# Optimization experiments

Measured on AMD Instinct MI355X. Metric: run time of the kernel, lower is better.

Reference implementation:

```python
import jax, jax.numpy as jnp
import numpy as np

N_QUBITS = 12
DIM = 2 ** N_QUBITS
BATCH = 2048


def setup_inputs() -> dict:
    key = jax.random.key(0)
    k1, k2, k3 = jax.random.split(key, 3)
    inputs = jax.random.normal(k1, (BATCH, N_QUBITS), dtype=jnp.float32)
    weight = jax.random.normal(k2, (3 + 2 * N_QUBITS,), dtype=jnp.float32)
    entangle_matrix = jax.random.normal(k3, (DIM, DIM), dtype=jnp.float32)
    return {"inputs": inputs, "weight": weight, "entangle_matrix": entangle_matrix}


def _encode(ry_angles, rz_angles):
    # Encoder: state = prod over qubits of first column of (Rz*Ry) per qubit.
    ry = ry_angles / 2
    rz = rz_angles / 2
    a = jnp.cos(ry) * jnp.exp(-1j * rz)  # entry11 (row bit = 0)
    b = jnp.sin(ry) * jnp.exp(1j * rz)   # entry21 (row bit = 1)
    col2 = jnp.stack([a, b], axis=-1).astype(jnp.complex64)  # [B, n, 2]
    B, n = ry.shape
    v = jnp.ones((B, 1), dtype=jnp.complex64)
    for q in range(n):  # Kronecker fold over qubits (big-endian, matches dec2bin)
        v = (v[:, :, None] * col2[:, q][:, None, :]).reshape(B, -1)
    return v  # [B, 2^n]


def _rot_mat(w):
    # rot_mat: per-qubit Rx(w[q]) @ Rz(w[n+q]), then full Kronecker product.
    n = w.shape[0] // 2
    tx = (w[:n] / 2).astype(jnp.complex64)
    tz = (w[n:] / 2).astype(jnp.complex64)
    c, s = jnp.cos(tx), jnp.sin(tx)
    rx = jnp.stack([jnp.stack([c, -1j * s], -1),
                    jnp.stack([-1j * s, c], -1)], -2)  # [n,2,2]
    ez = jnp.exp(-1j * tz)
    zero = jnp.zeros_like(ez)
    rz = jnp.stack([jnp.stack([ez, zero], -1),
                    jnp.stack([zero, jnp.exp(1j * tz)], -1)], -2)  # [n,2,2]
    mats = jnp.einsum('qij,qjk->qik', rx, rz)
    M = mats[0]
    for q in range(1, n):
        M = jnp.kron(M, mats[q])
    return M  # [2^n, 2^n]


def _ry2(theta):
    a = theta / 2
    c, s = jnp.cos(a), jnp.sin(a)
    return jnp.stack([jnp.stack([c, -s]), jnp.stack([s, c])])  # [2,2] real


def _final_rot(th3):
    # final_rot_mat: Rz-form @ Ry-form @ Rx-form (all ry_mat_list), kron with identity.
    rot = _ry2(th3[2]) @ (_ry2(th3[1]) @ _ry2(th3[0]))
    eye = jnp.eye(DIM // 2, dtype=jnp.complex64)
    return jnp.kron(rot.astype(jnp.complex64), eye)  # [DIM, DIM]


def reference(inputs, weight, entangle_matrix):
    # initial=False branch
    ry_angles = inputs
    rz_angles = jnp.square(inputs)
    v = _encode(ry_angles, rz_angles)                 # [B, DIM] complex64
    E = entangle_matrix.astype(jnp.complex64)
    R = _rot_mat(weight[3:])
    M = E @ R @ E                                     # [DIM, DIM]
    v = v @ M.T                                       # tensordot dims ([-1],[-1])
    F = _final_rot(weight[:3])
    v = v @ F.T
    half = DIM // 2
    # vector[:, half:] = 0 then sum |.|^2  <=>  sum over first half
    return jnp.sum(jnp.square(jnp.abs(v[:, :half])), axis=-1)  # [B] float32
```

## Files before the change

kernel.cpp:

```cpp
#include <hip/hip_runtime.h>
#include <math.h>

#define QDIM 4096
#define NQ 12
#define QBATCH 2048

typedef _Float16 f16x8 __attribute__((ext_vector_type(8)));
typedef float f32x4 __attribute__((ext_vector_type(4)));
typedef int i32x4 __attribute__((ext_vector_type(4)));

__device__ __forceinline__ void gld_lds16(const void* gptr, void* ldsptr) {
    __builtin_amdgcn_global_load_lds(
        (const __attribute__((address_space(1))) void*)gptr,
        (__attribute__((address_space(3))) void*)ldsptr,
        16, 0, 0);
}

__device__ __forceinline__ int q8(float x) {
    float y = fminf(fmaxf(x, -127.f), 127.f);
    return (int)rintf(y);
}
__device__ __forceinline__ int pack4_i8(int a, int b, int c, int d) {
    return (a & 0xFF) | ((b & 0xFF) << 8) | ((c & 0xFF) << 16) | ((d & 0xFF) << 24);
}

__global__ __launch_bounds__(256) void conv_kernel(
    const float* __restrict__ E, const float* __restrict__ wgt,
    _Float16* __restrict__ Eh, signed char* __restrict__ G8)
{
    float th = 0.5f * (wgt[0] + wgt[1] + wgt[2]);
    float c0 = cosf(th), c1 = -sinf(th);
    const float qs = 127.f / 6.f;
    size_t flat = ((size_t)blockIdx.x * 256 + threadIdx.x) * 8;
    size_t n = flat >> 12;
    size_t k = flat & (QDIM - 1);
    const float* p0 = E + n * QDIM + k;
    const float* p1 = p0 + (size_t)QBATCH * QDIM;
    float4 a0 = ((const float4*)p0)[0], a1 = ((const float4*)p0)[1];
    float4 b0 = ((const float4*)p1)[0], b1 = ((const float4*)p1)[1];
    f16x8 h0 = { (_Float16)a0.x, (_Float16)a0.y, (_Float16)a0.z, (_Float16)a0.w,
                 (_Float16)a1.x, (_Float16)a1.y, (_Float16)a1.z, (_Float16)a1.w };
    f16x8 h1 = { (_Float16)b0.x, (_Float16)b0.y, (_Float16)b0.z, (_Float16)b0.w,
                 (_Float16)b1.x, (_Float16)b1.y, (_Float16)b1.z, (_Float16)b1.w };
    *(f16x8*)&Eh[n * QDIM + k] = h0;
    *(f16x8*)&Eh[(n + QBATCH) * QDIM + k] = h1;
    float g[8] = { c0*a0.x + c1*b0.x, c0*a0.y + c1*b0.y, c0*a0.z + c1*b0.z, c0*a0.w + c1*b0.w,
                   c0*a1.x + c1*b1.x, c0*a1.y + c1*b1.y, c0*a1.z + c1*b1.z, c0*a1.w + c1*b1.w };
    int2 gp = { pack4_i8(q8(g[0]*qs), q8(g[1]*qs), q8(g[2]*qs), q8(g[3]*qs)),
                pack4_i8(q8(g[4]*qs), q8(g[5]*qs), q8(g[6]*qs), q8(g[7]*qs)) };
    *(int2*)&G8[n * QDIM + k] = gp;
}

__global__ __launch_bounds__(256) void expand_kernel(
    const float* __restrict__ inputs, _Float16* __restrict__ A1,
    float* __restrict__ out)
{
    __shared__ float ab[NQ][4];
    const int b = blockIdx.x;
    const int tid = threadIdx.x;
    if (tid == 0) out[b] = 0.f;
    if (tid < NQ) {
        float x = inputs[b * NQ + tid];
        float ry = 0.5f * x;
        float rz = 0.5f * x * x;
        float ca = cosf(ry), sa = sinf(ry), cz = cosf(rz), sz = sinf(rz);
        ab[tid][0] = ca * cz;  ab[tid][1] = -ca * sz;
        ab[tid][2] = sa * cz;  ab[tid][3] =  sa * sz;
    }
    __syncthreads();
    float pr0 = 1.f, pi0 = 0.f;
#pragma unroll
    for (int q = 0; q < 8; ++q) {
        int bit = (tid >> (7 - q)) & 1;
        float cr = ab[q][bit * 2 + 0], ci = ab[q][bit * 2 + 1];
        float nr = pr0 * cr - pi0 * ci;
        float ni = pr0 * ci + pi0 * cr;
        pr0 = nr; pi0 = ni;
    }
    f16x8 vr[2], vi[2];
#pragma unroll
    for (int u = 0; u < 16; ++u) {
        float pr = pr0, pi = pi0;
#pragma unroll
        for (int q = 8; q < 12; ++q) {
            int bit = (u >> (11 - q)) & 1;
            float cr = ab[q][bit * 2 + 0], ci = ab[q][bit * 2 + 1];
            float nr = pr * cr - pi * ci;
            float ni = pr * ci + pi * cr;
            pr = nr; pi = ni;
        }
        vr[u >> 3][u & 7] = (_Float16)pr;
        vi[u >> 3][u & 7] = (_Float16)pi;
    }
    const int idx0 = tid * 16;
    *(f16x8*)&A1[(size_t)b * QDIM + idx0] = vr[0];
    *(f16x8*)&A1[(size_t)b * QDIM + idx0 + 8] = vr[1];
    *(f16x8*)&A1[(size_t)(b + QBATCH) * QDIM + idx0] = vi[0];
    *(f16x8*)&A1[(size_t)(b + QBATCH) * QDIM + idx0 + 8] = vi[1];
}

__global__ __launch_bounds__(256) void gemm_f16(
    const _Float16* __restrict__ A, const _Float16* __restrict__ B,
    _Float16* __restrict__ C, int N)
{
    const int K = QDIM;
    __shared__ __attribute__((aligned(16))) _Float16 As[128 * 64];
    __shared__ __attribute__((aligned(16))) _Float16 Bs[128 * 64];

    const int tid  = threadIdx.x;
    const int wave = tid >> 6;
    const int lane = tid & 63;
    const int bn0 = blockIdx.x * 128;
    const int bm0 = blockIdx.y * 128;
    const int wm = (wave >> 1) * 64;
    const int wn = (wave & 1) * 64;
    const int q = lane >> 4;
    const int r = lane & 15;
    const int rx = r & 7;

    f32x4 acc[4][4];
#pragma unroll
    for (int i = 0; i < 4; ++i)
#pragma unroll
        for (int j = 0; j < 4; ++j) acc[i][j] = (f32x4){0.f, 0.f, 0.f, 0.f};

    const _Float16* gA[4];
    const _Float16* gB[4];
    char* lA[4];
    char* lB[4];
#pragma unroll
    for (int n = 0; n < 4; ++n) {
        int c = n * 256 + tid;
        int row = c >> 3;
        int gcol = (c & 7) ^ (row & 7);
        gA[n] = A + (size_t)(bm0 + row) * K + gcol * 8;
        gB[n] = B + (size_t)(bn0 + row) * K + gcol * 8;
        lA[n] = (char*)As + (n * 256 + wave * 64) * 16;
        lB[n] = (char*)Bs + (n * 256 + wave * 64) * 16;
    }

    for (int kk = 0; kk < K; kk += 64) {
#pragma unroll
        for (int n = 0; n < 4; ++n) {
            gld_lds16(gA[n] + kk, lA[n]);
            gld_lds16(gB[n] + kk, lB[n]);
        }
        __syncthreads();

#pragma unroll
        for (int s = 0; s < 2; ++s) {
            f16x8 af[4], bf[4];
#pragma unroll
            for (int i = 0; i < 4; ++i) {
                int row = wm + i * 16 + r;
                af[i] = *(const f16x8*)&As[(row * 8 + ((s * 4 + q) ^ rx)) * 8];
            }
#pragma unroll
            for (int j = 0; j < 4; ++j) {
                int row = wn + j * 16 + r;
                bf[j] = *(const f16x8*)&Bs[(row * 8 + ((s * 4 + q) ^ rx)) * 8];
            }
#pragma unroll
            for (int i = 0; i < 4; ++i)
#pragma unroll
                for (int j = 0; j < 4; ++j)
                    acc[i][j] = __builtin_amdgcn_mfma_f32_16x16x32_f16(af[i], bf[j], acc[i][j], 0, 0, 0);
        }
        __syncthreads();
    }

#pragma unroll
    for (int i = 0; i < 4; ++i) {
        const int crow = bm0 + wm + i * 16 + q * 4;
#pragma unroll
        for (int rr = 0; rr < 4; ++rr)
#pragma unroll
            for (int j = 0; j < 4; ++j)
                C[(size_t)(crow + rr) * N + bn0 + wn + j * 16 + r] = (_Float16)acc[i][j][rr];
    }
}

__global__ __launch_bounds__(256) void butterfly_kernel(
    const _Float16* __restrict__ u1, const float* __restrict__ wgt,
    signed char* __restrict__ A2, float* __restrict__ scaleA)
{
    __shared__ float sRe[4366];
    __shared__ float sIm[4366];
    __shared__ float mats[NQ][8];
    __shared__ float red[8];
    const int blk = blockIdx.x;
    const int tid = threadIdx.x;
    const int ah = tid >> 4;
    const int al = tid & 15;

    if (tid < NQ) {
        float tx = 0.5f * wgt[3 + tid];
        float tz = 0.5f * wgt[15 + tid];
        float c = cosf(tx), s = sinf(tx), cz = cosf(tz), sz = sinf(tz);
        mats[tid][0] =  c * cz;  mats[tid][1] = -c * sz;
        mats[tid][2] =  s * sz;  mats[tid][3] = -s * cz;
        mats[tid][4] = -s * sz;  mats[tid][5] = -s * cz;
        mats[tid][6] =  c * cz;  mats[tid][7] =  c * sz;
    }

    float xr[16], xi[16];
    {
        const _Float16* pRe = u1 + (size_t)blk * QDIM + tid * 16;
        const _Float16* pIm = u1 + (size_t)(blk + QBATCH) * QDIM + tid * 16;
        f16x8 r0 = ((const f16x8*)pRe)[0], r1 = ((const f16x8*)pRe)[1];
        f16x8 i0 = ((const f16x8*)pIm)[0], i1 = ((const f16x8*)pIm)[1];
#pragma unroll
        for (int j = 0; j < 8; ++j) {
            xr[j] = (float)r0[j]; xr[8 + j] = (float)r1[j];
            xi[j] = (float)i0[j]; xi[8 + j] = (float)i1[j];
        }
    }
    __syncthreads();

#define BFLY_STAGE(arrR, arrI, K_, Q_)                                         \
    {                                                                          \
        const float m00r = mats[Q_][0], m00i = mats[Q_][1];                    \
        const float m01r = mats[Q_][2], m01i = mats[Q_][3];                    \
        const float m10r = mats[Q_][4], m10i = mats[Q_][5];                    \
        const float m11r = mats[Q_][6], m11i = mats[Q_][7];                    \
        _Pragma("unroll")                                                      \
        for (int t = 0; t < 8; ++t) {                                          \
            int i0 = ((t >> (K_)) << ((K_) + 1)) | (t & ((1 << (K_)) - 1));    \
            int i1 = i0 | (1 << (K_));                                         \
            float x0r = arrR[i0], x0i = arrI[i0];                              \
            float x1r = arrR[i1], x1i = arrI[i1];                              \
            arrR[i0] = m00r * x0r - m00i * x0i + m01r * x1r - m01i * x1i;      \
            arrI[i0] = m00r * x0i + m00i * x0r + m01r * x1i + m01i * x1r;      \
            arrR[i1] = m10r * x0r - m10i * x0i + m11r * x1r - m11i * x1i;      \
            arrI[i1] = m10r * x0i + m10i * x0r + m11r * x1i + m11i * x1r;      \
        }                                                                      \
    }

#pragma unroll
    for (int p = 0; p < 4; ++p) BFLY_STAGE(xr, xi, p, 11 - p);

#pragma unroll
    for (int c = 0; c < 16; ++c) {
        sRe[273 * ah + 17 * al + c] = xr[c];
        sIm[273 * ah + 17 * al + c] = xi[c];
    }
    __syncthreads();

    float yr[16], yi[16];
#pragma unroll
    for (int b = 0; b < 16; ++b) {
        yr[b] = sRe[273 * ah + 17 * b + al];
        yi[b] = sIm[273 * ah + 17 * b + al];
    }
#pragma unroll
    for (int p = 0; p < 4; ++p) BFLY_STAGE(yr, yi, p, 7 - p);

#pragma unroll
    for (int b = 0; b < 16; ++b) {
        sRe[273 * ah + 17 * b + al] = yr[b];
        sIm[273 * ah + 17 * b + al] = yi[b];
    }
    __syncthreads();

    float zr[16], zi[16];
#pragma unroll
    for (int a = 0; a < 16; ++a) {
        zr[a] = sRe[273 * a + 17 * ah + al];
        zi[a] = sIm[273 * a + 17 * ah + al];
    }
#pragma unroll
    for (int p = 0; p < 4; ++p) BFLY_STAGE(zr, zi, p, 3 - p);

    float mR = 0.f, mI = 0.f;
#pragma unroll
    for (int j = 0; j < 16; ++j) {
        mR = fmaxf(mR, fabsf(zr[j]));
        mI = fmaxf(mI, fabsf(zi[j]));
    }
#pragma unroll
    for (int off = 32; off > 0; off >>= 1) {
        mR = fmaxf(mR, __shfl_xor(mR, off, 64));
        mI = fmaxf(mI, __shfl_xor(mI, off, 64));
    }
    const int wid = tid >> 6;
    if ((tid & 63) == 0) { red[wid] = mR; red[4 + wid] = mI; }
    __syncthreads();
    mR = fmaxf(fmaxf(red[0], red[1]), fmaxf(red[2], red[3]));
    mI = fmaxf(fmaxf(red[4], red[5]), fmaxf(red[6], red[7]));
    mR = fmaxf(mR, 1e-30f);
    mI = fmaxf(mI, 1e-30f);
    if (tid == 0) {
        scaleA[blk] = mR / 127.f;
        scaleA[blk + QBATCH] = mI / 127.f;
    }
    const float invR = 127.f / mR, invI = 127.f / mI;

    signed char* oRe = A2 + (size_t)blk * QDIM + ah * 16 + al;
    signed char* oIm = A2 + (size_t)(blk + QBATCH) * QDIM + ah * 16 + al;
#pragma unroll
    for (int a = 0; a < 16; ++a) {
        oRe[a * 256] = (signed char)q8(zr[a] * invR);
        oIm[a * 256] = (signed char)q8(zi[a] * invI);
    }
#undef BFLY_STAGE
}

__global__ __launch_bounds__(256) void gemm2_i8(
    const signed char* __restrict__ A, const signed char* __restrict__ B,
    const float* __restrict__ scaleA, float* __restrict__ out)
{
    const int K = QDIM;
    __shared__ __attribute__((aligned(16))) signed char As[128 * 128];
    __shared__ __attribute__((aligned(16))) signed char Bs[128 * 128];

    const int tid  = threadIdx.x;
    const int wave = tid >> 6;
    const int lane = tid & 63;
    const int bn0 = blockIdx.x * 128;
    const int bm0 = blockIdx.y * 128;
    const int wm = (wave >> 1) * 64;
    const int wn = (wave & 1) * 64;
    const int q = lane >> 4;
    const int r = lane & 15;
    const int rx = r & 7;

    i32x4 acc[4][4];
#pragma unroll
    for (int i = 0; i < 4; ++i)
#pragma unroll
        for (int j = 0; j < 4; ++j) acc[i][j] = (i32x4){0, 0, 0, 0};

    const signed char* gA[4];
    const signed char* gB[4];
    char* lA[4];
    char* lB[4];
#pragma unroll
    for (int n = 0; n < 4; ++n) {
        int c = n * 256 + tid;
        int row = c >> 3;
        int gcol = (c & 7) ^ (row & 7);
        gA[n] = A + (size_t)(bm0 + row) * K + gcol * 16;
        gB[n] = B + (size_t)(bn0 + row) * K + gcol * 16;
        lA[n] = (char*)As + (n * 256 + wave * 64) * 16;
        lB[n] = (char*)Bs + (n * 256 + wave * 64) * 16;
    }

    for (int kk = 0; kk < K; kk += 128) {
#pragma unroll
        for (int n = 0; n < 4; ++n) {
            gld_lds16(gA[n] + kk, lA[n]);
            gld_lds16(gB[n] + kk, lB[n]);
        }
        __syncthreads();

#pragma unroll
        for (int s = 0; s < 2; ++s) {
            i32x4 af[4], bf[4];
#pragma unroll
            for (int i = 0; i < 4; ++i) {
                int row = wm + i * 16 + r;
                af[i] = *(const i32x4*)&As[row * 128 + (((s * 4 + q) ^ rx) * 16)];
            }
#pragma unroll
            for (int j = 0; j < 4; ++j) {
                int row = wn + j * 16 + r;
                bf[j] = *(const i32x4*)&Bs[row * 128 + (((s * 4 + q) ^ rx) * 16)];
            }
#pragma unroll
            for (int i = 0; i < 4; ++i)
#pragma unroll
                for (int j = 0; j < 4; ++j)
                    acc[i][j] = __builtin_amdgcn_mfma_i32_16x16x64_i8(af[i], bf[j], acc[i][j], 0, 0, 0);
        }
        __syncthreads();
    }

    const float dqG = 6.f / 127.f;
#pragma unroll
    for (int i = 0; i < 4; ++i) {
#pragma unroll
        for (int rr = 0; rr < 4; ++rr) {
            const int row = bm0 + wm + i * 16 + q * 4 + rr;
            const float sc = scaleA[row] * dqG;
            float v = 0.f;
#pragma unroll
            for (int j = 0; j < 4; ++j) {
                float t = sc * (float)acc[i][j][rr];
                v = fmaf(t, t, v);
            }
            v += __shfl_xor(v, 1, 64);
            v += __shfl_xor(v, 2, 64);
            v += __shfl_xor(v, 4, 64);
            v += __shfl_xor(v, 8, 64);
            if (r == 0) atomicAdd(&out[row & (QBATCH - 1)], v);
        }
    }
}

extern "C" void kernel_launch(void* const* d_in, const int* in_sizes, int n_in,
                              void* d_out, int out_size, void* d_ws, size_t ws_size,
                              hipStream_t stream)
{
    const float* inputs = (const float*)d_in[0];
    const float* weight = (const float*)d_in[1];
    const float* E      = (const float*)d_in[2];
    float* out = (float*)d_out;

    char* ws = (char*)d_ws;
    const size_t MB = 1024 * 1024;
    _Float16*    Eh     = (_Float16*)   (ws + 0);
    signed char* G8     = (signed char*)(ws + 32 * MB);
    _Float16*    A1     = (_Float16*)   (ws + 40 * MB);
    _Float16*    u1     = (_Float16*)   (ws + 72 * MB);
    signed char* A2     = (signed char*)(ws + 104 * MB);
    float*       scaleA = (float*)      (ws + 120 * MB);

    conv_kernel<<<(QBATCH * QDIM / 8) / 256, 256, 0, stream>>>(E, weight, Eh, G8);
    expand_kernel<<<QBATCH, 256, 0, stream>>>(inputs, A1, out);
    gemm_f16<<<dim3(QDIM / 128, QDIM / 128), 256, 0, stream>>>(A1, Eh, u1, QDIM);
    butterfly_kernel<<<QBATCH, 256, 0, stream>>>(u1, weight, A2, scaleA);
    gemm2_i8<<<dim3(2048 / 128, QDIM / 128), 256, 0, stream>>>(A2, G8, scaleA, out);
}
```

Measured before the change: 321.4 us.

## Switch both GEMMs to 32x32 MFMA tiles and merge prep kernels

```diff
diff --git a/kernel.cpp b/kernel.cpp
--- a/kernel.cpp
+++ b/kernel.cpp
@@ -6,8 +6,9 @@
 #define QBATCH 2048
 
 typedef _Float16 f16x8 __attribute__((ext_vector_type(8)));
-typedef float f32x4 __attribute__((ext_vector_type(4)));
+typedef float f32x16 __attribute__((ext_vector_type(16)));
 typedef int i32x4 __attribute__((ext_vector_type(4)));
+typedef int i32x16 __attribute__((ext_vector_type(16)));
 
 __device__ __forceinline__ void gld_lds16(const void* gptr, void* ldsptr) {
     __builtin_amdgcn_global_load_lds(
@@ -24,82 +25,81 @@
     return (a & 0xFF) | ((b & 0xFF) << 8) | ((c & 0xFF) << 16) | ((d & 0xFF) << 24);
 }
 
-__global__ __launch_bounds__(256) void conv_kernel(
-    const float* __restrict__ E, const float* __restrict__ wgt,
-    _Float16* __restrict__ Eh, signed char* __restrict__ G8)
+__global__ __launch_bounds__(256) void prep_kernel(
+    const float* __restrict__ E, const float* __restrict__ inputs,
+    const float* __restrict__ wgt,
+    _Float16* __restrict__ Eh, signed char* __restrict__ G8,
+    _Float16* __restrict__ A1, float* __restrict__ out)
 {
-    float th = 0.5f * (wgt[0] + wgt[1] + wgt[2]);
-    float c0 = cosf(th), c1 = -sinf(th);
-    const float qs = 127.f / 6.f;
-    size_t flat = ((size_t)blockIdx.x * 256 + threadIdx.x) * 8;
-    size_t n = flat >> 12;
-    size_t k = flat & (QDIM - 1);
-    const float* p0 = E + n * QDIM + k;
-    const float* p1 = p0 + (size_t)QBATCH * QDIM;
-    float4 a0 = ((const float4*)p0)[0], a1 = ((const float4*)p0)[1];
-    float4 b0 = ((const float4*)p1)[0], b1 = ((const float4*)p1)[1];
-    f16x8 h0 = { (_Float16)a0.x, (_Float16)a0.y, (_Float16)a0.z, (_Float16)a0.w,
-                 (_Float16)a1.x, (_Float16)a1.y, (_Float16)a1.z, (_Float16)a1.w };
-    f16x8 h1 = { (_Float16)b0.x, (_Float16)b0.y, (_Float16)b0.z, (_Float16)b0.w,
-                 (_Float16)b1.x, (_Float16)b1.y, (_Float16)b1.z, (_Float16)b1.w };
-    *(f16x8*)&Eh[n * QDIM + k] = h0;
-    *(f16x8*)&Eh[(n + QBATCH) * QDIM + k] = h1;
-    float g[8] = { c0*a0.x + c1*b0.x, c0*a0.y + c1*b0.y, c0*a0.z + c1*b0.z, c0*a0.w + c1*b0.w,
-                   c0*a1.x + c1*b1.x, c0*a1.y + c1*b1.y, c0*a1.z + c1*b1.z, c0*a1.w + c1*b1.w };
-    int2 gp = { pack4_i8(q8(g[0]*qs), q8(g[1]*qs), q8(g[2]*qs), q8(g[3]*qs)),
-                pack4_i8(q8(g[4]*qs), q8(g[5]*qs), q8(g[6]*qs), q8(g[7]*qs)) };
-    *(int2*)&G8[n * QDIM + k] = gp;
-}
-
-__global__ __launch_bounds__(256) void expand_kernel(
-    const float* __restrict__ inputs, _Float16* __restrict__ A1,
-    float* __restrict__ out)
-{
-    __shared__ float ab[NQ][4];
-    const int b = blockIdx.x;
     const int tid = threadIdx.x;
-    if (tid == 0) out[b] = 0.f;
-    if (tid < NQ) {
-        float x = inputs[b * NQ + tid];
-        float ry = 0.5f * x;
-        float rz = 0.5f * x * x;
-        float ca = cosf(ry), sa = sinf(ry), cz = cosf(rz), sz = sinf(rz);
-        ab[tid][0] = ca * cz;  ab[tid][1] = -ca * sz;
-        ab[tid][2] = sa * cz;  ab[tid][3] =  sa * sz;
-    }
-    __syncthreads();
-    float pr0 = 1.f, pi0 = 0.f;
-#pragma unroll
-    for (int q = 0; q < 8; ++q) {
-        int bit = (tid >> (7 - q)) & 1;
-        float cr = ab[q][bit * 2 + 0], ci = ab[q][bit * 2 + 1];
-        float nr = pr0 * cr - pi0 * ci;
-        float ni = pr0 * ci + pi0 * cr;
-        pr0 = nr; pi0 = ni;
-    }
-    f16x8 vr[2], vi[2];
-#pragma unroll
-    for (int u = 0; u < 16; ++u) {
-        float pr = pr0, pi = pi0;
-#pragma unroll
-        for (int q = 8; q < 12; ++q) {
-            int bit = (u >> (11 - q)) & 1;
+    if (blockIdx.x < 4096) {
+        float th = 0.5f * (wgt[0] + wgt[1] + wgt[2]);
+        float c0 = cosf(th), c1 = -sinf(th);
+        const float qs = 127.f / 6.f;
+        size_t flat = ((size_t)blockIdx.x * 256 + tid) * 8;
+        size_t n = flat >> 12;
+        size_t k = flat & (QDIM - 1);
+        const float* p0 = E + n * QDIM + k;
+        const float* p1 = p0 + (size_t)QBATCH * QDIM;
+        float4 a0 = ((const float4*)p0)[0], a1 = ((const float4*)p0)[1];
+        float4 b0 = ((const float4*)p1)[0], b1 = ((const float4*)p1)[1];
+        f16x8 h0 = { (_Float16)a0.x, (_Float16)a0.y, (_Float16)a0.z, (_Float16)a0.w,
+                     (_Float16)a1.x, (_Float16)a1.y, (_Float16)a1.z, (_Float16)a1.w };
+        f16x8 h1 = { (_Float16)b0.x, (_Float16)b0.y, (_Float16)b0.z, (_Float16)b0.w,
+                     (_Float16)b1.x, (_Float16)b1.y, (_Float16)b1.z, (_Float16)b1.w };
+        *(f16x8*)&Eh[n * QDIM + k] = h0;
+        *(f16x8*)&Eh[(n + QBATCH) * QDIM + k] = h1;
+        float g[8] = { c0*a0.x + c1*b0.x, c0*a0.y + c1*b0.y, c0*a0.z + c1*b0.z, c0*a0.w + c1*b0.w,
+                       c0*a1.x + c1*b1.x, c0*a1.y + c1*b1.y, c0*a1.z + c1*b1.z, c0*a1.w + c1*b1.w };
+        int2 gp = { pack4_i8(q8(g[0]*qs), q8(g[1]*qs), q8(g[2]*qs), q8(g[3]*qs)),
+                    pack4_i8(q8(g[4]*qs), q8(g[5]*qs), q8(g[6]*qs), q8(g[7]*qs)) };
+        *(int2*)&G8[n * QDIM + k] = gp;
+    } else {
+        __shared__ float ab[NQ][4];
+        const int b = blockIdx.x - 4096;
+        if (tid == 0) out[b] = 0.f;
+        if (tid < NQ) {
+            float x = inputs[b * NQ + tid];
+            float ry = 0.5f * x;
+            float rz = 0.5f * x * x;
+            float ca = cosf(ry), sa = sinf(ry), cz = cosf(rz), sz = sinf(rz);
+            ab[tid][0] = ca * cz;  ab[tid][1] = -ca * sz;
+            ab[tid][2] = sa * cz;  ab[tid][3] =  sa * sz;
+        }
+        __syncthreads();
+        float pr0 = 1.f, pi0 = 0.f;
+#pragma unroll
+        for (int q = 0; q < 8; ++q) {
+            int bit = (tid >> (7 - q)) & 1;
             float cr = ab[q][bit * 2 + 0], ci = ab[q][bit * 2 + 1];
-            float nr = pr * cr - pi * ci;
-            float ni = pr * ci + pi * cr;
-            pr = nr; pi = ni;
-        }
-        vr[u >> 3][u & 7] = (_Float16)pr;
-        vi[u >> 3][u & 7] = (_Float16)pi;
-    }
-    const int idx0 = tid * 16;
-    *(f16x8*)&A1[(size_t)b * QDIM + idx0] = vr[0];
-    *(f16x8*)&A1[(size_t)b * QDIM + idx0 + 8] = vr[1];
-    *(f16x8*)&A1[(size_t)(b + QBATCH) * QDIM + idx0] = vi[0];
-    *(f16x8*)&A1[(size_t)(b + QBATCH) * QDIM + idx0 + 8] = vi[1];
-}
-
-__global__ __launch_bounds__(256) void gemm_f16(
+            float nr = pr0 * cr - pi0 * ci;
+            float ni = pr0 * ci + pi0 * cr;
+            pr0 = nr; pi0 = ni;
+        }
+        f16x8 vr[2], vi[2];
+#pragma unroll
+        for (int u = 0; u < 16; ++u) {
+            float pr = pr0, pi = pi0;
+#pragma unroll
+            for (int q = 8; q < 12; ++q) {
+                int bit = (u >> (11 - q)) & 1;
+                float cr = ab[q][bit * 2 + 0], ci = ab[q][bit * 2 + 1];
+                float nr = pr * cr - pi * ci;
+                float ni = pr * ci + pi * cr;
+                pr = nr; pi = ni;
+            }
+            vr[u >> 3][u & 7] = (_Float16)pr;
+            vi[u >> 3][u & 7] = (_Float16)pi;
+        }
+        const int idx0 = tid * 16;
+        *(f16x8*)&A1[(size_t)b * QDIM + idx0] = vr[0];
+        *(f16x8*)&A1[(size_t)b * QDIM + idx0 + 8] = vr[1];
+        *(f16x8*)&A1[(size_t)(b + QBATCH) * QDIM + idx0] = vi[0];
+        *(f16x8*)&A1[(size_t)(b + QBATCH) * QDIM + idx0 + 8] = vi[1];
+    }
+}
+
+__global__ __launch_bounds__(256, 4) void gemm_f16(
     const _Float16* __restrict__ A, const _Float16* __restrict__ B,
     _Float16* __restrict__ C, int N)
 {
@@ -114,15 +114,17 @@
     const int bm0 = blockIdx.y * 128;
     const int wm = (wave >> 1) * 64;
     const int wn = (wave & 1) * 64;
-    const int q = lane >> 4;
-    const int r = lane & 15;
-    const int rx = r & 7;
-
-    f32x4 acc[4][4];
-#pragma unroll
-    for (int i = 0; i < 4; ++i)
-#pragma unroll
-        for (int j = 0; j < 4; ++j) acc[i][j] = (f32x4){0.f, 0.f, 0.f, 0.f};
+    const int rl = lane & 31;
+    const int kh = lane >> 5;
+    const int rx = rl & 7;
+
+    f32x16 acc[2][2];
+#pragma unroll
+    for (int i = 0; i < 2; ++i)
+#pragma unroll
+        for (int j = 0; j < 2; ++j)
+#pragma unroll
+            for (int e = 0; e < 16; ++e) acc[i][j][e] = 0.f;
 
     const _Float16* gA[4];
     const _Float16* gB[4];
@@ -148,36 +150,36 @@
         __syncthreads();
 
 #pragma unroll
-        for (int s = 0; s < 2; ++s) {
-            f16x8 af[4], bf[4];
-#pragma unroll
-            for (int i = 0; i < 4; ++i) {
-                int row = wm + i * 16 + r;
-                af[i] = *(const f16x8*)&As[(row * 8 + ((s * 4 + q) ^ rx)) * 8];
-            }
-#pragma unroll
-            for (int j = 0; j < 4; ++j) {
-                int row = wn + j * 16 + r;
-                bf[j] = *(const f16x8*)&Bs[(row * 8 + ((s * 4 + q) ^ rx)) * 8];
-            }
-#pragma unroll
-            for (int i = 0; i < 4; ++i)
-#pragma unroll
-                for (int j = 0; j < 4; ++j)
-                    acc[i][j] = __builtin_amdgcn_mfma_f32_16x16x32_f16(af[i], bf[j], acc[i][j], 0, 0, 0);
+        for (int s = 0; s < 4; ++s) {
+            f16x8 af[2], bf[2];
+#pragma unroll
+            for (int t = 0; t < 2; ++t) {
+                int row = wm + t * 32 + rl;
+                af[t] = *(const f16x8*)&As[row * 64 + ((2 * s + kh) ^ rx) * 8];
+            }
+#pragma unroll
+            for (int u = 0; u < 2; ++u) {
+                int row = wn + u * 32 + rl;
+                bf[u] = *(const f16x8*)&Bs[row * 64 + ((2 * s + kh) ^ rx) * 8];
+            }
+#pragma unroll
+            for (int t = 0; t < 2; ++t)
+#pragma unroll
+                for (int u = 0; u < 2; ++u)
+                    acc[t][u] = __builtin_amdgcn_mfma_f32_32x32x16_f16(af[t], bf[u], acc[t][u], 0, 0, 0);
         }
         __syncthreads();
     }
 
 #pragma unroll
-    for (int i = 0; i < 4; ++i) {
-        const int crow = bm0 + wm + i * 16 + q * 4;
-#pragma unroll
-        for (int rr = 0; rr < 4; ++rr)
-#pragma unroll
-            for (int j = 0; j < 4; ++j)
-                C[(size_t)(crow + rr) * N + bn0 + wn + j * 16 + r] = (_Float16)acc[i][j][rr];
-    }
+    for (int t = 0; t < 2; ++t)
+#pragma unroll
+        for (int reg = 0; reg < 16; ++reg) {
+            const int row = bm0 + wm + t * 32 + (reg & 3) + 8 * (reg >> 2) + 4 * kh;
+#pragma unroll
+            for (int u = 0; u < 2; ++u)
+                C[(size_t)row * N + bn0 + wn + u * 32 + rl] = (_Float16)acc[t][u][reg];
+        }
 }
 
 __global__ __launch_bounds__(256) void butterfly_kernel(
@@ -320,15 +322,17 @@
     const int bm0 = blockIdx.y * 128;
     const int wm = (wave >> 1) * 64;
     const int wn = (wave & 1) * 64;
-    const int q = lane >> 4;
-    const int r = lane & 15;
-    const int rx = r & 7;
-
-    i32x4 acc[4][4];
-#pragma unroll
-    for (int i = 0; i < 4; ++i)
-#pragma unroll
-        for (int j = 0; j < 4; ++j) acc[i][j] = (i32x4){0, 0, 0, 0};
+    const int rl = lane & 31;
+    const int kh = lane >> 5;
+    const int rx = rl & 7;
+
+    i32x16 acc[2][2];
+#pragma unroll
+    for (int i = 0; i < 2; ++i)
+#pragma unroll
+        for (int j = 0; j < 2; ++j)
+#pragma unroll
+            for (int e = 0; e < 16; ++e) acc[i][j][e] = 0;
 
     const signed char* gA[4];
     const signed char* gB[4];
@@ -354,47 +358,47 @@
         __syncthreads();
 
 #pragma unroll
-        for (int s = 0; s < 2; ++s) {
-            i32x4 af[4], bf[4];
-#pragma unroll
-            for (int i = 0; i < 4; ++i) {
-                int row = wm + i * 16 + r;
-                af[i] = *(const i32x4*)&As[row * 128 + (((s * 4 + q) ^ rx) * 16)];
-            }
-#pragma unroll
-            for (int j = 0; j < 4; ++j) {
-                int row = wn + j * 16 + r;
-                bf[j] = *(const i32x4*)&Bs[row * 128 + (((s * 4 + q) ^ rx) * 16)];
-            }
-#pragma unroll
-            for (int i = 0; i < 4; ++i)
-#pragma unroll
-                for (int j = 0; j < 4; ++j)
-                    acc[i][j] = __builtin_amdgcn_mfma_i32_16x16x64_i8(af[i], bf[j], acc[i][j], 0, 0, 0);
+        for (int s = 0; s < 4; ++s) {
+            i32x4 af[2], bf[2];
+#pragma unroll
+            for (int t = 0; t < 2; ++t) {
+                int row = wm + t * 32 + rl;
+                af[t] = *(const i32x4*)&As[row * 128 + (((2 * s + kh) ^ rx) * 16)];
+            }
+#pragma unroll
+            for (int u = 0; u < 2; ++u) {
+                int row = wn + u * 32 + rl;
+                bf[u] = *(const i32x4*)&Bs[row * 128 + (((2 * s + kh) ^ rx) * 16)];
+            }
+#pragma unroll
+            for (int t = 0; t < 2; ++t)
+#pragma unroll
+                for (int u = 0; u < 2; ++u)
+                    acc[t][u] = __builtin_amdgcn_mfma_i32_32x32x32_i8(af[t], bf[u], acc[t][u], 0, 0, 0);
         }
         __syncthreads();
     }
 
     const float dqG = 6.f / 127.f;
 #pragma unroll
-    for (int i = 0; i < 4; ++i) {
-#pragma unroll
-        for (int rr = 0; rr < 4; ++rr) {
-            const int row = bm0 + wm + i * 16 + q * 4 + rr;
+    for (int t = 0; t < 2; ++t)
+#pragma unroll
+        for (int reg = 0; reg < 16; ++reg) {
+            const int row = bm0 + wm + t * 32 + (reg & 3) + 8 * (reg >> 2) + 4 * kh;
             const float sc = scaleA[row] * dqG;
             float v = 0.f;
 #pragma unroll
-            for (int j = 0; j < 4; ++j) {
-                float t = sc * (float)acc[i][j][rr];
-                v = fmaf(t, t, v);
+            for (int u = 0; u < 2; ++u) {
+                float tt = sc * (float)acc[t][u][reg];
+                v = fmaf(tt, tt, v);
             }
             v += __shfl_xor(v, 1, 64);
             v += __shfl_xor(v, 2, 64);
             v += __shfl_xor(v, 4, 64);
             v += __shfl_xor(v, 8, 64);
-            if (r == 0) atomicAdd(&out[row & (QBATCH - 1)], v);
-        }
-    }
+            v += __shfl_xor(v, 16, 64);
+            if (rl == 0) atomicAdd(&out[row & (QBATCH - 1)], v);
+        }
 }
 
 extern "C" void kernel_launch(void* const* d_in, const int* in_sizes, int n_in,
@@ -415,8 +419,7 @@
     signed char* A2     = (signed char*)(ws + 104 * MB);
     float*       scaleA = (float*)      (ws + 120 * MB);
 
-    conv_kernel<<<(QBATCH * QDIM / 8) / 256, 256, 0, stream>>>(E, weight, Eh, G8);
-    expand_kernel<<<QBATCH, 256, 0, stream>>>(inputs, A1, out);
+    prep_kernel<<<4096 + 2048, 256, 0, stream>>>(E, inputs, weight, Eh, G8, A1, out);
     gemm_f16<<<dim3(QDIM / 128, QDIM / 128), 256, 0, stream>>>(A1, Eh, u1, QDIM);
     butterfly_kernel<<<QBATCH, 256, 0, stream>>>(u1, weight, A2, scaleA);
     gemm2_i8<<<dim3(2048 / 128, QDIM / 128), 256, 0, stream>>>(A2, G8, scaleA, out);
```

New measurement: 349.0 us. 8.6% more time.

## Fuse prep kernels and load GEMM A operands directly from global into registers

Applied to the files above, without the earlier changes.

```diff
diff --git a/kernel.cpp b/kernel.cpp
--- a/kernel.cpp
+++ b/kernel.cpp
@@ -24,79 +24,78 @@
     return (a & 0xFF) | ((b & 0xFF) << 8) | ((c & 0xFF) << 16) | ((d & 0xFF) << 24);
 }
 
-__global__ __launch_bounds__(256) void conv_kernel(
-    const float* __restrict__ E, const float* __restrict__ wgt,
-    _Float16* __restrict__ Eh, signed char* __restrict__ G8)
+__global__ __launch_bounds__(256) void prep_kernel(
+    const float* __restrict__ E, const float* __restrict__ inputs,
+    const float* __restrict__ wgt,
+    _Float16* __restrict__ Eh, signed char* __restrict__ G8,
+    _Float16* __restrict__ A1, float* __restrict__ out)
 {
-    float th = 0.5f * (wgt[0] + wgt[1] + wgt[2]);
-    float c0 = cosf(th), c1 = -sinf(th);
-    const float qs = 127.f / 6.f;
-    size_t flat = ((size_t)blockIdx.x * 256 + threadIdx.x) * 8;
-    size_t n = flat >> 12;
-    size_t k = flat & (QDIM - 1);
-    const float* p0 = E + n * QDIM + k;
-    const float* p1 = p0 + (size_t)QBATCH * QDIM;
-    float4 a0 = ((const float4*)p0)[0], a1 = ((const float4*)p0)[1];
-    float4 b0 = ((const float4*)p1)[0], b1 = ((const float4*)p1)[1];
-    f16x8 h0 = { (_Float16)a0.x, (_Float16)a0.y, (_Float16)a0.z, (_Float16)a0.w,
-                 (_Float16)a1.x, (_Float16)a1.y, (_Float16)a1.z, (_Float16)a1.w };
-    f16x8 h1 = { (_Float16)b0.x, (_Float16)b0.y, (_Float16)b0.z, (_Float16)b0.w,
-                 (_Float16)b1.x, (_Float16)b1.y, (_Float16)b1.z, (_Float16)b1.w };
-    *(f16x8*)&Eh[n * QDIM + k] = h0;
-    *(f16x8*)&Eh[(n + QBATCH) * QDIM + k] = h1;
-    float g[8] = { c0*a0.x + c1*b0.x, c0*a0.y + c1*b0.y, c0*a0.z + c1*b0.z, c0*a0.w + c1*b0.w,
-                   c0*a1.x + c1*b1.x, c0*a1.y + c1*b1.y, c0*a1.z + c1*b1.z, c0*a1.w + c1*b1.w };
-    int2 gp = { pack4_i8(q8(g[0]*qs), q8(g[1]*qs), q8(g[2]*qs), q8(g[3]*qs)),
-                pack4_i8(q8(g[4]*qs), q8(g[5]*qs), q8(g[6]*qs), q8(g[7]*qs)) };
-    *(int2*)&G8[n * QDIM + k] = gp;
-}
-
-__global__ __launch_bounds__(256) void expand_kernel(
-    const float* __restrict__ inputs, _Float16* __restrict__ A1,
-    float* __restrict__ out)
-{
-    __shared__ float ab[NQ][4];
-    const int b = blockIdx.x;
     const int tid = threadIdx.x;
-    if (tid == 0) out[b] = 0.f;
-    if (tid < NQ) {
-        float x = inputs[b * NQ + tid];
-        float ry = 0.5f * x;
-        float rz = 0.5f * x * x;
-        float ca = cosf(ry), sa = sinf(ry), cz = cosf(rz), sz = sinf(rz);
-        ab[tid][0] = ca * cz;  ab[tid][1] = -ca * sz;
-        ab[tid][2] = sa * cz;  ab[tid][3] =  sa * sz;
-    }
-    __syncthreads();
-    float pr0 = 1.f, pi0 = 0.f;
-#pragma unroll
-    for (int q = 0; q < 8; ++q) {
-        int bit = (tid >> (7 - q)) & 1;
-        float cr = ab[q][bit * 2 + 0], ci = ab[q][bit * 2 + 1];
-        float nr = pr0 * cr - pi0 * ci;
-        float ni = pr0 * ci + pi0 * cr;
-        pr0 = nr; pi0 = ni;
-    }
-    f16x8 vr[2], vi[2];
-#pragma unroll
-    for (int u = 0; u < 16; ++u) {
-        float pr = pr0, pi = pi0;
-#pragma unroll
-        for (int q = 8; q < 12; ++q) {
-            int bit = (u >> (11 - q)) & 1;
+    if (blockIdx.x < 4096) {
+        float th = 0.5f * (wgt[0] + wgt[1] + wgt[2]);
+        float c0 = cosf(th), c1 = -sinf(th);
+        const float qs = 127.f / 6.f;
+        size_t flat = ((size_t)blockIdx.x * 256 + tid) * 8;
+        size_t n = flat >> 12;
+        size_t k = flat & (QDIM - 1);
+        const float* p0 = E + n * QDIM + k;
+        const float* p1 = p0 + (size_t)QBATCH * QDIM;
+        float4 a0 = ((const float4*)p0)[0], a1 = ((const float4*)p0)[1];
+        float4 b0 = ((const float4*)p1)[0], b1 = ((const float4*)p1)[1];
+        f16x8 h0 = { (_Float16)a0.x, (_Float16)a0.y, (_Float16)a0.z, (_Float16)a0.w,
+                     (_Float16)a1.x, (_Float16)a1.y, (_Float16)a1.z, (_Float16)a1.w };
+        f16x8 h1 = { (_Float16)b0.x, (_Float16)b0.y, (_Float16)b0.z, (_Float16)b0.w,
+                     (_Float16)b1.x, (_Float16)b1.y, (_Float16)b1.z, (_Float16)b1.w };
+        *(f16x8*)&Eh[n * QDIM + k] = h0;
+        *(f16x8*)&Eh[(n + QBATCH) * QDIM + k] = h1;
+        float g[8] = { c0*a0.x + c1*b0.x, c0*a0.y + c1*b0.y, c0*a0.z + c1*b0.z, c0*a0.w + c1*b0.w,
+                       c0*a1.x + c1*b1.x, c0*a1.y + c1*b1.y, c0*a1.z + c1*b1.z, c0*a1.w + c1*b1.w };
+        int2 gp = { pack4_i8(q8(g[0]*qs), q8(g[1]*qs), q8(g[2]*qs), q8(g[3]*qs)),
+                    pack4_i8(q8(g[4]*qs), q8(g[5]*qs), q8(g[6]*qs), q8(g[7]*qs)) };
+        *(int2*)&G8[n * QDIM + k] = gp;
+    } else {
+        __shared__ float ab[NQ][4];
+        const int b = blockIdx.x - 4096;
+        if (tid == 0) out[b] = 0.f;
+        if (tid < NQ) {
+            float x = inputs[b * NQ + tid];
+            float ry = 0.5f * x;
+            float rz = 0.5f * x * x;
+            float ca = cosf(ry), sa = sinf(ry), cz = cosf(rz), sz = sinf(rz);
+            ab[tid][0] = ca * cz;  ab[tid][1] = -ca * sz;
+            ab[tid][2] = sa * cz;  ab[tid][3] =  sa * sz;
+        }
+        __syncthreads();
+        float pr0 = 1.f, pi0 = 0.f;
+#pragma unroll
+        for (int q = 0; q < 8; ++q) {
+            int bit = (tid >> (7 - q)) & 1;
             float cr = ab[q][bit * 2 + 0], ci = ab[q][bit * 2 + 1];
-            float nr = pr * cr - pi * ci;
-            float ni = pr * ci + pi * cr;
-            pr = nr; pi = ni;
-        }
-        vr[u >> 3][u & 7] = (_Float16)pr;
-        vi[u >> 3][u & 7] = (_Float16)pi;
-    }
-    const int idx0 = tid * 16;
-    *(f16x8*)&A1[(size_t)b * QDIM + idx0] = vr[0];
-    *(f16x8*)&A1[(size_t)b * QDIM + idx0 + 8] = vr[1];
-    *(f16x8*)&A1[(size_t)(b + QBATCH) * QDIM + idx0] = vi[0];
-    *(f16x8*)&A1[(size_t)(b + QBATCH) * QDIM + idx0 + 8] = vi[1];
+            float nr = pr0 * cr - pi0 * ci;
+            float ni = pr0 * ci + pi0 * cr;
+            pr0 = nr; pi0 = ni;
+        }
+        f16x8 vr[2], vi[2];
+#pragma unroll
+        for (int u = 0; u < 16; ++u) {
+            float pr = pr0, pi = pi0;
+#pragma unroll
+            for (int q = 8; q < 12; ++q) {
+                int bit = (u >> (11 - q)) & 1;
+                float cr = ab[q][bit * 2 + 0], ci = ab[q][bit * 2 + 1];
+                float nr = pr * cr - pi * ci;
+                float ni = pr * ci + pi * cr;
+                pr = nr; pi = ni;
+            }
+            vr[u >> 3][u & 7] = (_Float16)pr;
+            vi[u >> 3][u & 7] = (_Float16)pi;
+        }
+        const int idx0 = tid * 16;
+        *(f16x8*)&A1[(size_t)b * QDIM + idx0] = vr[0];
+        *(f16x8*)&A1[(size_t)b * QDIM + idx0 + 8] = vr[1];
+        *(f16x8*)&A1[(size_t)(b + QBATCH) * QDIM + idx0] = vi[0];
+        *(f16x8*)&A1[(size_t)(b + QBATCH) * QDIM + idx0 + 8] = vi[1];
+    }
 }
 
 __global__ __launch_bounds__(256) void gemm_f16(
@@ -104,7 +103,6 @@
     _Float16* __restrict__ C, int N)
 {
     const int K = QDIM;
-    __shared__ __attribute__((aligned(16))) _Float16 As[128 * 64];
     __shared__ __attribute__((aligned(16))) _Float16 Bs[128 * 64];
 
     const int tid  = threadIdx.x;
@@ -124,37 +122,36 @@
 #pragma unroll
         for (int j = 0; j < 4; ++j) acc[i][j] = (f32x4){0.f, 0.f, 0.f, 0.f};
 
-    const _Float16* gA[4];
     const _Float16* gB[4];
-    char* lA[4];
     char* lB[4];
 #pragma unroll
     for (int n = 0; n < 4; ++n) {
         int c = n * 256 + tid;
         int row = c >> 3;
         int gcol = (c & 7) ^ (row & 7);
-        gA[n] = A + (size_t)(bm0 + row) * K + gcol * 8;
         gB[n] = B + (size_t)(bn0 + row) * K + gcol * 8;
-        lA[n] = (char*)As + (n * 256 + wave * 64) * 16;
         lB[n] = (char*)Bs + (n * 256 + wave * 64) * 16;
     }
+    const _Float16* pA[4];
+#pragma unroll
+    for (int i = 0; i < 4; ++i)
+        pA[i] = A + (size_t)(bm0 + wm + i * 16 + r) * K + q * 8;
 
     for (int kk = 0; kk < K; kk += 64) {
 #pragma unroll
-        for (int n = 0; n < 4; ++n) {
-            gld_lds16(gA[n] + kk, lA[n]);
+        for (int n = 0; n < 4; ++n)
             gld_lds16(gB[n] + kk, lB[n]);
-        }
+        f16x8 af[2][4];
+#pragma unroll
+        for (int s = 0; s < 2; ++s)
+#pragma unroll
+            for (int i = 0; i < 4; ++i)
+                af[s][i] = *(const f16x8*)(pA[i] + kk + s * 32);
         __syncthreads();
 
 #pragma unroll
         for (int s = 0; s < 2; ++s) {
-            f16x8 af[4], bf[4];
-#pragma unroll
-            for (int i = 0; i < 4; ++i) {
-                int row = wm + i * 16 + r;
-                af[i] = *(const f16x8*)&As[(row * 8 + ((s * 4 + q) ^ rx)) * 8];
-            }
+            f16x8 bf[4];
 #pragma unroll
             for (int j = 0; j < 4; ++j) {
                 int row = wn + j * 16 + r;
@@ -164,7 +161,7 @@
             for (int i = 0; i < 4; ++i)
 #pragma unroll
                 for (int j = 0; j < 4; ++j)
-                    acc[i][j] = __builtin_amdgcn_mfma_f32_16x16x32_f16(af[i], bf[j], acc[i][j], 0, 0, 0);
+                    acc[i][j] = __builtin_amdgcn_mfma_f32_16x16x32_f16(af[s][i], bf[j], acc[i][j], 0, 0, 0);
         }
         __syncthreads();
     }
@@ -310,7 +307,6 @@
     const float* __restrict__ scaleA, float* __restrict__ out)
 {
     const int K = QDIM;
-    __shared__ __attribute__((aligned(16))) signed char As[128 * 128];
     __shared__ __attribute__((aligned(16))) signed char Bs[128 * 128];
 
     const int tid  = threadIdx.x;
@@ -330,37 +326,36 @@
 #pragma unroll
         for (int j = 0; j < 4; ++j) acc[i][j] = (i32x4){0, 0, 0, 0};
 
-    const signed char* gA[4];
     const signed char* gB[4];
-    char* lA[4];
     char* lB[4];
 #pragma unroll
     for (int n = 0; n < 4; ++n) {
         int c = n * 256 + tid;
         int row = c >> 3;
         int gcol = (c & 7) ^ (row & 7);
-        gA[n] = A + (size_t)(bm0 + row) * K + gcol * 16;
         gB[n] = B + (size_t)(bn0 + row) * K + gcol * 16;
-        lA[n] = (char*)As + (n * 256 + wave * 64) * 16;
         lB[n] = (char*)Bs + (n * 256 + wave * 64) * 16;
     }
+    const signed char* pA[4];
+#pragma unroll
+    for (int i = 0; i < 4; ++i)
+        pA[i] = A + (size_t)(bm0 + wm + i * 16 + r) * K + q * 16;
 
     for (int kk = 0; kk < K; kk += 128) {
 #pragma unroll
-        for (int n = 0; n < 4; ++n) {
-            gld_lds16(gA[n] + kk, lA[n]);
+        for (int n = 0; n < 4; ++n)
             gld_lds16(gB[n] + kk, lB[n]);
-        }
+        i32x4 af[2][4];
+#pragma unroll
+        for (int s = 0; s < 2; ++s)
+#pragma unroll
+            for (int i = 0; i < 4; ++i)
+                af[s][i] = *(const i32x4*)(pA[i] + kk + s * 64);
         __syncthreads();
 
 #pragma unroll
         for (int s = 0; s < 2; ++s) {
-            i32x4 af[4], bf[4];
-#pragma unroll
-            for (int i = 0; i < 4; ++i) {
-                int row = wm + i * 16 + r;
-                af[i] = *(const i32x4*)&As[row * 128 + (((s * 4 + q) ^ rx) * 16)];
-            }
+            i32x4 bf[4];
 #pragma unroll
             for (int j = 0; j < 4; ++j) {
                 int row = wn + j * 16 + r;
@@ -370,7 +365,7 @@
             for (int i = 0; i < 4; ++i)
 #pragma unroll
                 for (int j = 0; j < 4; ++j)
-                    acc[i][j] = __builtin_amdgcn_mfma_i32_16x16x64_i8(af[i], bf[j], acc[i][j], 0, 0, 0);
+                    acc[i][j] = __builtin_amdgcn_mfma_i32_16x16x64_i8(af[s][i], bf[j], acc[i][j], 0, 0, 0);
         }
         __syncthreads();
     }
@@ -415,8 +410,7 @@
     signed char* A2     = (signed char*)(ws + 104 * MB);
     float*       scaleA = (float*)      (ws + 120 * MB);
 
-    conv_kernel<<<(QBATCH * QDIM / 8) / 256, 256, 0, stream>>>(E, weight, Eh, G8);
-    expand_kernel<<<QBATCH, 256, 0, stream>>>(inputs, A1, out);
+    prep_kernel<<<4096 + 2048, 256, 0, stream>>>(E, inputs, weight, Eh, G8, A1, out);
     gemm_f16<<<dim3(QDIM / 128, QDIM / 128), 256, 0, stream>>>(A1, Eh, u1, QDIM);
     butterfly_kernel<<<QBATCH, 256, 0, stream>>>(u1, weight, A2, scaleA);
     gemm2_i8<<<dim3(2048 / 128, QDIM / 128), 256, 0, stream>>>(A2, G8, scaleA, out);
```

After: 492.7 us. 53.3% more time.
